# Kernel tuning notes

Hardware: AMD Instinct MI355X
Metric: run time of the kernel (lower is better)

## Reference

```python
import jax, jax.numpy as jnp
import numpy as np

N, E, F_IN, F_E, H, HEADS, NG = 50000, 300000, 16, 8, 64, 4, 64
D_HEAD = H // HEADS
EPS = 1e-5


def setup_inputs() -> dict:
    key = jax.random.key(0)
    ks = jax.random.split(key, 12)
    def rn(k, shape, s=0.1):
        return jax.random.normal(k, shape, jnp.float32) * s
    return dict(
        x=jax.random.normal(ks[0], (N, F_IN), jnp.float32),
        edge_index=jax.random.randint(ks[1], (2, E), 0, N),
        edge_attr=jax.random.normal(ks[2], (E, F_E), jnp.float32),
        batch=jnp.sort(jax.random.randint(ks[3], (N,), 0, NG)),
        # edge_net: Linear(F_E, H*F_IN) -> ReLU -> Linear(H*F_IN, H*F_IN)
        en_w1=rn(ks[4], (F_E, H * F_IN)), en_b1=jnp.zeros((H * F_IN,), jnp.float32),
        en_w2=rn(ks[5], (H * F_IN, H * F_IN)), en_b2=jnp.zeros((H * F_IN,), jnp.float32),
        # NNConv root weight + bias
        root_w=rn(ks[6], (F_IN, H)), conv1_b=jnp.zeros((H,), jnp.float32),
        norm1_w=jnp.ones((H,), jnp.float32), norm1_b=jnp.zeros((H,), jnp.float32),
        # GATConv: lin weight, attention vectors, bias
        gat_w=rn(ks[7], (H, H)),
        att_src=rn(ks[8], (HEADS, D_HEAD)), att_dst=rn(ks[9], (HEADS, D_HEAD)),
        gat_b=jnp.zeros((H,), jnp.float32),
        norm2_w=jnp.ones((H,), jnp.float32), norm2_b=jnp.zeros((H,), jnp.float32),
        lin_w=rn(ks[10], (H, 1)), lin_b=jnp.zeros((1,), jnp.float32),
    )


def _graph_layernorm(x, w, b):
    # PyG LayerNorm(mode='graph') with batch=None: scalar mean/std over ALL elems
    mu = x.mean()
    sd = jnp.sqrt(((x - mu) ** 2).mean())
    return (x - mu) / (sd + EPS) * w + b


def reference(x, edge_index, edge_attr, batch, en_w1, en_b1, en_w2, en_b2,
              root_w, conv1_b, norm1_w, norm1_b, gat_w, att_src, att_dst,
              gat_b, norm2_w, norm2_b, lin_w, lin_b):
    src, dst = edge_index[0], edge_index[1]
    # --- NNConv: per-edge weight matrices from edge_net ---
    w_e = jax.nn.relu(edge_attr @ en_w1 + en_b1) @ en_w2 + en_b2
    w_e = w_e.reshape(E, F_IN, H)                      # [E, in, out]
    msg = jnp.einsum('ef,efh->eh', x[src], w_e)        # gather-matmul per edge
    agg = jax.ops.segment_sum(msg, dst, num_segments=N)
    deg = jax.ops.segment_sum(jnp.ones((E,), x.dtype), dst, num_segments=N)
    agg = agg / jnp.maximum(deg, 1.0)[:, None]         # aggr='mean'
    h = x @ root_w + agg + conv1_b
    h = jax.nn.relu(h)
    h = _graph_layernorm(h, norm1_w, norm1_b)
    # dropout: eval mode -> identity
    # --- GATConv (edge_attr=None at call site; add self-loops, softmax attn) ---
    loops = jnp.arange(N)
    s2 = jnp.concatenate([src, loops])
    d2 = jnp.concatenate([dst, loops])
    xh = (h @ gat_w).reshape(N, HEADS, D_HEAD)
    a_src = (xh * att_src).sum(-1)                     # [N, HEADS]
    a_dst = (xh * att_dst).sum(-1)
    alpha = jax.nn.leaky_relu(a_src[s2] + a_dst[d2], 0.2)  # [E+N, HEADS]
    amax = jax.ops.segment_max(alpha, d2, num_segments=N)
    alpha = jnp.exp(alpha - amax[d2])
    asum = jax.ops.segment_sum(alpha, d2, num_segments=N)
    alpha = alpha / (asum[d2] + 1e-16)
    out = jax.ops.segment_sum(alpha[:, :, None] * xh[s2], d2, num_segments=N)
    h2 = out.reshape(N, H) + gat_b                     # concat heads
    h2 = jax.nn.relu(h2)
    h2 = _graph_layernorm(h2, norm2_w, norm2_b)
    # --- global mean pool + linear head ---
    gs = jax.ops.segment_sum(h2, batch, num_segments=NG)
    cnt = jax.ops.segment_sum(jnp.ones((N,), h2.dtype), batch, num_segments=NG)
    pooled = gs / jnp.maximum(cnt, 1.0)[:, None]
    return pooled @ lin_w + lin_b                      # [NG, 1]
```

## Files before the change

### kernel.cpp

```cpp
#include <hip/hip_runtime.h>
#include <hip/hip_bf16.h>

#define N_NODES 50000
#define E_EDGES 300000
#define NGRAPH 64
#define KTOT 16512
#define KC 128
#define NCHUNK 129
#define CSPLIT 65
#define NEGRP 1172
#define LNEPS 1e-5f
#define NBLK_N 196
#define NBLK_P 12500
#define RPRE 1.00146484375f

typedef __bf16 bf16x8 __attribute__((ext_vector_type(8)));
typedef float floatx4 __attribute__((ext_vector_type(4)));
typedef float f32x2 __attribute__((ext_vector_type(2)));
typedef unsigned int u32x4 __attribute__((ext_vector_type(4)));

__device__ __forceinline__ void async_load16(const void* g, void* l) {
  __builtin_amdgcn_global_load_lds(
      (__attribute__((address_space(1))) void*)g,
      (__attribute__((address_space(3))) void*)l, 16, 0, 0);
}

__device__ __forceinline__ unsigned pkt(f32x2 p) {
  return __builtin_amdgcn_perm(__float_as_uint(p[1]), __float_as_uint(p[0]), 0x07060302u);
}
__device__ __forceinline__ unsigned pkbf(float a, float b) {
  unsigned ua = __float_as_uint(a) + 0x8000u;
  unsigned ub = __float_as_uint(b) + 0x8000u;
  return __builtin_amdgcn_perm(ub, ua, 0x07060302u);
}

__global__ void k_prep(const float* __restrict__ w2, const float* __restrict__ b2,
                       __bf16* __restrict__ Tt) {
  __shared__ float tile[64][65];
  int t = threadIdx.x;
  int kf0 = blockIdx.x * 64;
  int r4 = t >> 6;
  int cc = t & 63;
#pragma unroll
  for (int p = 0; p < 16; ++p) {
    int row = p * 4 + r4;
    int kf = kf0 + row;
    float v = 0.f;
    if (kf < 16384) {
      int k = kf >> 4, f = kf & 15;
      v = w2[k * 1024 + f * 64 + cc];
    } else if (kf < 16400) {
      v = b2[(kf - 16384) * 64 + cc];
    }
    tile[row][cc] = v;
  }
  __syncthreads();
#pragma unroll
  for (int p = 0; p < 16; ++p) {
    int h = p * 4 + r4;
    Tt[(size_t)h * KTOT + kf0 + cc] = (__bf16)tile[cc][h];
  }
}

__global__ void k_prepw(const float* __restrict__ w1, float* __restrict__ W1t) {
  int i = blockIdx.x * 256 + threadIdx.x;
  if (i < 8192) { int k = i >> 3, j = i & 7; W1t[i] = w1[j * 1024 + k]; }
}

__global__ void k_cnt(const int* __restrict__ ei, int* __restrict__ degI) {
  int e = blockIdx.x * 256 + threadIdx.x;
  if (e < E_EDGES) atomicAdd(&degI[ei[E_EDGES + e]], 1);
}

__global__ void k_scanA(const int* __restrict__ degI, int* __restrict__ bsum) {
  __shared__ int sm[256];
  int t = threadIdx.x;
  int i = blockIdx.x * 256 + t;
  sm[t] = (i < N_NODES) ? degI[i] : 0;
  __syncthreads();
  for (int off = 128; off > 0; off >>= 1) {
    if (t < off) sm[t] += sm[t + off];
    __syncthreads();
  }
  if (t == 0) bsum[blockIdx.x] = sm[0];
}

__global__ void k_scanB(const int* __restrict__ bsum, int* __restrict__ bpre) {
  __shared__ int s[256];
  int t = threadIdx.x;
  int v = (t < NBLK_N) ? bsum[t] : 0;
  s[t] = v;
  __syncthreads();
  for (int off = 1; off < 256; off <<= 1) {
    int add = (t >= off) ? s[t - off] : 0;
    __syncthreads();
    s[t] += add;
    __syncthreads();
  }
  if (t < NBLK_N) bpre[t] = s[t] - v;
}

__global__ void k_scanC(const int* __restrict__ degI, const int* __restrict__ bpre,
                        int* __restrict__ rowptr, int* __restrict__ cursor) {
  __shared__ int s[256];
  int t = threadIdx.x;
  int i = blockIdx.x * 256 + t;
  int d = (i < N_NODES) ? degI[i] : 0;
  s[t] = d;
  __syncthreads();
  for (int off = 1; off < 256; off <<= 1) {
    int add = (t >= off) ? s[t - off] : 0;
    __syncthreads();
    s[t] += add;
    __syncthreads();
  }
  int r = bpre[blockIdx.x] + s[t] - d;
  if (i < N_NODES) {
    rowptr[i] = r;
    cursor[i] = r;
    if (i == N_NODES - 1) rowptr[N_NODES] = r + d;
  }
}

__global__ void k_scatter(const int* __restrict__ ei, int* __restrict__ cursor,
                          int* __restrict__ colsrc) {
  int e = blockIdx.x * 256 + threadIdx.x;
  if (e < E_EDGES) {
    int s = ei[e], d = ei[E_EDGES + e];
    int pos = atomicAdd(&cursor[d], 1);
    colsrc[pos] = s;
  }
}

__global__ __launch_bounds__(256, 3)
void k_nnconv(const float* __restrict__ x, const int* __restrict__ ei,
              const float* __restrict__ ea, const float* __restrict__ W1t,
              const float* __restrict__ b1, const __bf16* __restrict__ Tt,
              float* __restrict__ agg) {
  __shared__ __align__(16) __bf16 sB[2][64 * KC];
  __shared__ int sSrc[256];
  __shared__ int sDst[256];

  const int tid = threadIdx.x;
  const int wv = tid >> 6;
  const int lane = tid & 63;
  const int l15 = lane & 15;
  const int quad = lane >> 4;
  const int qxl = quad ^ l15;
  const bool qhi = (lane & 32) != 0;
  const unsigned rsel = qhi ? 0x07060100u : 0x05040100u;
  const int grp = blockIdx.x >> 1;
  const int half = blockIdx.x & 1;
  const int cstart = half ? CSPLIT : 0;
  const int cend = half ? NCHUNK : CSPLIT;
  const int base = grp * 256;

  int e = base + tid;
  bool valid = e < E_EDGES;
  sSrc[tid] = valid ? ei[e] : 0;
  sDst[tid] = valid ? ei[E_EDGES + e] : -1;

  f32x2 ea2[4];
  {
    const float4* p = (const float4*)(ea + (size_t)(valid ? e : 0) * 8);
    float4 a0 = p[0], a1 = p[1];
    ea2[0] = (f32x2){a0.x, a0.y};
    ea2[1] = (f32x2){a0.z, a0.w};
    ea2[2] = (f32x2){a1.x, a1.y};
    ea2[3] = (f32x2){a1.z, a1.w};
  }
  __syncthreads();

  const int f0 = (quad & 1) * 8;
  f32x2 xf2[4][4];
#pragma unroll
  for (int mb = 0; mb < 4; ++mb) {
    int el = wv * 64 + mb * 16 + l15;
    const float4* px = (const float4*)(x + (size_t)sSrc[el] * 16 + f0);
    float4 v0 = px[0], v1 = px[1];
    xf2[mb][0] = (f32x2){v0.x * RPRE, v0.y * RPRE};
    xf2[mb][1] = (f32x2){v0.z * RPRE, v0.w * RPRE};
    xf2[mb][2] = (f32x2){v1.x * RPRE, v1.y * RPRE};
    xf2[mb][3] = (f32x2){v1.z * RPRE, v1.w * RPRE};
  }

  int bpaddr[4];
#pragma unroll
  for (int mb = 0; mb < 4; ++mb) bpaddr[mb] = (mb * 16 + l15) * 4;

  const int tidh = tid >> 4;
  const int ccsw = (tid & 15) ^ (tidh & 15);
  const __bf16* gbase = Tt + (size_t)tidh * KTOT + ccsw * 8 + cstart * KC;

  auto stageB = [&](int buf) {
    const __bf16* p = gbase;
#pragma unroll
    for (int it = 0; it < 4; ++it) {
      async_load16(p, &sB[buf][(it * 256 + tid) * 8]);
      p += 16 * KTOT;
    }
    gbase += KC;
  };

  unsigned prr[4];
  auto calcR = [&](int c, const float* w1p, const float* b1p) {
    if (c < 128) {
#pragma unroll
      for (int ks = 0; ks < 4; ++ks) {
        float rv[2];
#pragma unroll
        for (int kk = 0; kk < 2; ++kk) {
          const f32x2* w = (const f32x2*)(w1p + (ks * 2 + kk) * 8);
          f32x2 s01 = ea2[0] * w[0] + ea2[1] * w[1];
          f32x2 s23 = ea2[2] * w[2] + ea2[3] * w[3];
          f32x2 s = s01 + s23;
          rv[kk] = fmaxf(b1p[ks * 2 + kk] + s[0] + s[1], 0.f);
        }
        prr[ks] = pkbf(rv[0], rv[1]);
      }
    } else {
      prr[0] = 0x00003F80u;
      prr[1] = prr[2] = prr[3] = 0u;
    }
  };

  unsigned ubuf[16];
  auto bcastR = [&]() {
#pragma unroll
    for (int ks = 0; ks < 4; ++ks)
#pragma unroll
      for (int mb = 0; mb < 4; ++mb)
        ubuf[ks * 4 + mb] = (unsigned)__builtin_amdgcn_ds_bpermute(bpaddr[mb], (int)prr[ks]);
  };

  floatx4 acc[4][4];
#pragma unroll
  for (int mb = 0; mb < 4; ++mb)
#pragma unroll
    for (int nb = 0; nb < 4; ++nb) acc[mb][nb] = floatx4{0.f, 0.f, 0.f, 0.f};

  stageB(0);
  calcR(cstart, W1t + cstart * 64, b1 + cstart * 8);
  bcastR();
  const float* w1p = W1t + (cstart + 1) * 64;
  const float* b1p = b1 + (cstart + 1) * 8;
  int buf = 0;
  for (int c = cstart; c < cend; ++c) {
    __syncthreads();
    if (c + 1 < cend) stageB(buf ^ 1);
    float rvc[16];
#pragma unroll
    for (int i = 0; i < 16; ++i)
      rvc[i] = __uint_as_float(__builtin_amdgcn_perm(ubuf[i], 0u, rsel));
#pragma unroll
    for (int ks = 0; ks < 4; ++ks) {
      int t1 = qxl ^ (ks * 4);
      bf16x8 bfr[4];
#pragma unroll
      for (int nb = 0; nb < 4; ++nb)
        bfr[nb] = *(const bf16x8*)&sB[buf][(nb * 16 + l15) * KC + t1 * 8];
#pragma unroll
      for (int mb = 0; mb < 4; ++mb) {
        float rv = rvc[ks * 4 + mb];
        f32x2 rv2 = {rv, rv};
        u32x4 U;
        U[0] = pkt(rv2 * xf2[mb][0]);
        U[1] = pkt(rv2 * xf2[mb][1]);
        U[2] = pkt(rv2 * xf2[mb][2]);
        U[3] = pkt(rv2 * xf2[mb][3]);
        bf16x8 A = __builtin_bit_cast(bf16x8, U);
#pragma unroll
        for (int nb = 0; nb < 4; ++nb)
          acc[mb][nb] = __builtin_amdgcn_mfma_f32_16x16x32_bf16(A, bfr[nb], acc[mb][nb], 0, 0, 0);
      }
    }
    if (c + 1 < cend) {
      calcR(c + 1, w1p, b1p);
      bcastR();
      w1p += 64; b1p += 8;
    }
    buf ^= 1;
  }

#pragma unroll
  for (int mb = 0; mb < 4; ++mb) {
    int el = wv * 64 + mb * 16 + quad * 4;
#pragma unroll
    for (int reg = 0; reg < 4; ++reg) {
      int dd = sDst[el + reg];
      if (dd >= 0) {
#pragma unroll
        for (int nb = 0; nb < 4; ++nb)
          atomicAdd(&agg[(size_t)dd * 64 + nb * 16 + l15], acc[mb][nb][reg]);
      }
    }
  }
}

__global__ void k_root(const float* __restrict__ x, const float* __restrict__ rootw,
                       const float* __restrict__ conv1b, const float* __restrict__ agg,
                       const int* __restrict__ degI, float* __restrict__ hpre,
                       float* __restrict__ rpart) {
  __shared__ float sW[1024];
  __shared__ float sx[64];
  __shared__ float red[8];
  int t = threadIdx.x;
  int blk = blockIdx.x;
#pragma unroll
  for (int i = 0; i < 4; ++i) sW[t + i * 256] = rootw[t + i * 256];
  if (t < 64) sx[t] = x[(size_t)blk * 64 + t];
  __syncthreads();
  int ln = t >> 6, h = t & 63;
  int n = blk * 4 + ln;
  float acc = conv1b[h];
#pragma unroll
  for (int f = 0; f < 16; ++f) acc += sx[ln * 16 + f] * sW[f * 64 + h];
  float dv = fmaxf((float)degI[n], 1.0f);
  float v = acc + agg[(size_t)n * 64 + h] / dv;
  v = fmaxf(v, 0.f);
  hpre[(size_t)n * 64 + h] = v;
  float s1 = v, s2 = v * v;
  for (int o = 32; o > 0; o >>= 1) { s1 += __shfl_down(s1, o); s2 += __shfl_down(s2, o); }
  if ((t & 63) == 0) { red[t >> 6] = s1; red[4 + (t >> 6)] = s2; }
  __syncthreads();
  if (t == 0) {
    rpart[blk * 2] = red[0] + red[1] + red[2] + red[3];
    rpart[blk * 2 + 1] = red[4] + red[5] + red[6] + red[7];
  }
}

__global__ void k_fold1(const float* __restrict__ rpart, const float* __restrict__ n1w,
                        const float* __restrict__ n1b, const float* __restrict__ gatw,
                        float* __restrict__ gw2, float* __restrict__ tb) {
  __shared__ float red[8];
  __shared__ float sMI[2];
  __shared__ float sS[64], sT[64];
  int t = threadIdx.x;
  int wv = t >> 6, lane = t & 63;
  float a = 0.f, b = 0.f;
  for (int i = t; i < NBLK_P; i += 256) { a += rpart[2 * i]; b += rpart[2 * i + 1]; }
  for (int o = 32; o > 0; o >>= 1) { a += __shfl_down(a, o); b += __shfl_down(b, o); }
  if (lane == 0) { red[wv] = a; red[4 + wv] = b; }
  __syncthreads();
  if (t == 0) {
    float A = red[0] + red[1] + red[2] + red[3];
    float B = red[4] + red[5] + red[6] + red[7];
    const float M = (float)N_NODES * 64.f;
    float mu = A / M;
    float var = fmaxf(B / M - mu * mu, 0.f);
    sMI[0] = mu;
    sMI[1] = 1.f / (sqrtf(var) + LNEPS);
  }
  __syncthreads();
  if (t < 64) {
    float mu = sMI[0], inv = sMI[1];
    sS[t] = inv * n1w[t];
    sT[t] = n1b[t] - mu * inv * n1w[t];
  }
  __syncthreads();
  if (t < 64) {
    float acc = 0.f;
    for (int i = 0; i < 64; ++i) {
      float g = gatw[i * 64 + t];
      gw2[i * 64 + t] = sS[i] * g;
      acc += sT[i] * g;
    }
    tb[t] = acc;
  }
}

__global__ void k_gatlin(const float* __restrict__ hpre, const float* __restrict__ gw2,
                         const float* __restrict__ tb, const float* __restrict__ attS,
                         const float* __restrict__ attD, float* __restrict__ xh,
                         float* __restrict__ asrc, float* __restrict__ adst) {
  __shared__ float sW[4096];
  __shared__ float sh[256];
  __shared__ float sxh[256];
  int t = threadIdx.x;
  int blk = blockIdx.x;
#pragma unroll
  for (int i = 0; i < 16; ++i) sW[t + i * 256] = gw2[t + i * 256];
  sh[t] = hpre[(size_t)blk * 256 + t];
  __syncthreads();
  int ln = t >> 6, h = t & 63;
  float acc = tb[h];
  for (int i = 0; i < 64; ++i) acc += sh[ln * 64 + i] * sW[i * 64 + h];
  xh[(size_t)blk * 256 + t] = acc;
  sxh[t] = acc;
  __syncthreads();
  if (t < 32) {
    int ln2 = t >> 3, rem = t & 7;
    int hd = rem & 3;
    const float* av = (rem >> 2) ? attD : attS;
    float a = 0.f;
#pragma unroll
    for (int d = 0; d < 16; ++d) a += sxh[ln2 * 64 + hd * 16 + d] * av[hd * 16 + d];
    int n = blk * 4 + ln2;
    if (rem >> 2) adst[n * 4 + hd] = a; else asrc[n * 4 + hd] = a;
  }
}

__global__ void k_gat(const int* __restrict__ rowptr, const int* __restrict__ colsrc,
                      const float* __restrict__ xh, const float* __restrict__ asrc,
                      const float* __restrict__ adst, const float* __restrict__ gatb,
                      float* __restrict__ act, float* __restrict__ gpart) {
  __shared__ float sP[4][256];
  __shared__ int sS[4][64];
  __shared__ float sRed[8];
  int t = threadIdx.x;
  int wv = t >> 6, lane = t & 63;
  int n = blockIdx.x * 4 + wv;
  int start = rowptr[n], end = rowptr[n + 1];
  int deg = end - start;
  int myhd = lane >> 4;
  float ad[4];
#pragma unroll
  for (int hd = 0; hd < 4; ++hd) ad[hd] = adst[n * 4 + hd];
  float m[4] = {-1e30f, -1e30f, -1e30f, -1e30f};
  float l[4] = {0.f, 0.f, 0.f, 0.f};
  float O = 0.f;
  int items = deg + 1;
  for (int t0 = 0; t0 < items; t0 += 64) {
    int cnt = min(64, items - t0);
    int idx = t0 + lane;
    bool has = lane < cnt;
    int s = n;
    if (has && idx < deg) s = colsrc[start + idx];
    float a[4];
#pragma unroll
    for (int hd = 0; hd < 4; ++hd) {
      float av = has ? (asrc[s * 4 + hd] + ad[hd]) : -1e30f;
      a[hd] = (av > 0.f) ? av : 0.2f * av;
    }
    float tm[4];
#pragma unroll
    for (int hd = 0; hd < 4; ++hd) tm[hd] = a[hd];
#pragma unroll
    for (int off = 32; off > 0; off >>= 1)
#pragma unroll
      for (int hd = 0; hd < 4; ++hd) tm[hd] = fmaxf(tm[hd], __shfl_xor(tm[hd], off));
    float p[4];
#pragma unroll
    for (int hd = 0; hd < 4; ++hd) {
      float mn = fmaxf(m[hd], tm[hd]);
      float sc = __expf(m[hd] - mn);
      l[hd] *= sc;
      if (hd == myhd) O *= sc;
      m[hd] = mn;
      p[hd] = has ? __expf(a[hd] - mn) : 0.f;
    }
    float ts[4];
#pragma unroll
    for (int hd = 0; hd < 4; ++hd) ts[hd] = p[hd];
#pragma unroll
    for (int off = 32; off > 0; off >>= 1)
#pragma unroll
      for (int hd = 0; hd < 4; ++hd) ts[hd] += __shfl_xor(ts[hd], off);
#pragma unroll
    for (int hd = 0; hd < 4; ++hd) l[hd] += ts[hd];
    sS[wv][lane] = s;
#pragma unroll
    for (int hd = 0; hd < 4; ++hd) sP[wv][lane * 4 + hd] = p[hd];
    for (int e2 = 0; e2 < cnt; ++e2) {
      int ss = sS[wv][e2];
      float pp = sP[wv][e2 * 4 + myhd];
      O = fmaf(pp, xh[(size_t)ss * 64 + lane], O);
    }
  }
  float lmy = (myhd & 2) ? ((myhd & 1) ? l[3] : l[2]) : ((myhd & 1) ? l[1] : l[0]);
  float outv = O / (lmy + 1e-16f);
  float v = fmaxf(outv + gatb[lane], 0.f);
  act[(size_t)n * 64 + lane] = v;
  float s1 = v, s2 = v * v;
#pragma unroll
  for (int off = 32; off > 0; off >>= 1) { s1 += __shfl_down(s1, off); s2 += __shfl_down(s2, off); }
  if (lane == 0) { sRed[wv] = s1; sRed[4 + wv] = s2; }
  __syncthreads();
  if (t == 0) {
    gpart[blockIdx.x * 2] = sRed[0] + sRed[1] + sRed[2] + sRed[3];
    gpart[blockIdx.x * 2 + 1] = sRed[4] + sRed[5] + sRed[6] + sRed[7];
  }
}

__global__ void k_fold2(const float* __restrict__ gpart, const float* __restrict__ n2w,
                        const float* __restrict__ n2b, const float* __restrict__ linw,
                        const float* __restrict__ linb, float* __restrict__ wl) {
  __shared__ float red[8];
  __shared__ float sMI[2];
  int t = threadIdx.x;
  int wv = t >> 6, lane = t & 63;
  float a = 0.f, b = 0.f;
  for (int i = t; i < NBLK_P; i += 256) { a += gpart[2 * i]; b += gpart[2 * i + 1]; }
  for (int o = 32; o > 0; o >>= 1) { a += __shfl_down(a, o); b += __shfl_down(b, o); }
  if (lane == 0) { red[wv] = a; red[4 + wv] = b; }
  __syncthreads();
  if (t == 0) {
    float A = red[0] + red[1] + red[2] + red[3];
    float B = red[4] + red[5] + red[6] + red[7];
    const float M = (float)N_NODES * 64.f;
    float mu = A / M;
    float var = fmaxf(B / M - mu * mu, 0.f);
    sMI[0] = mu;
    sMI[1] = 1.f / (sqrtf(var) + LNEPS);
  }
  __syncthreads();
  if (t < 64) {
    float mu = sMI[0], inv = sMI[1];
    float w = inv * n2w[t] * linw[t];
    float p = (n2b[t] - mu * inv * n2w[t]) * linw[t];
    wl[t] = w;
    for (int o = 32; o > 0; o >>= 1) p += __shfl_down(p, o);
    if (t == 0) wl[64] = p + linb[0];
  }
}

__global__ void k_out(const float* __restrict__ act, const float* __restrict__ wl,
                      const int* __restrict__ batch, float* __restrict__ out) {
  __shared__ float red[4];
  __shared__ float swl[64];
  int g = blockIdx.x;
  int t = threadIdx.x;
  int wv = t >> 6, lane = t & 63;
  if (t < 64) swl[t] = wl[t];
  __syncthreads();
  auto lbound = [&](int key) {
    int lo = 0, hi = N_NODES;
    while (lo < hi) { int mid = (lo + hi) >> 1; if (batch[mid] < key) lo = mid + 1; else hi = mid; }
    return lo;
  };
  int lo = lbound(g), hi = lbound(g + 1);
  int cntn = hi - lo;
  float s = 0.f;
  for (int idx = t; idx < cntn * 64; idx += 256) {
    int n = lo + (idx >> 6);
    int d = idx & 63;
    s += act[(size_t)n * 64 + d] * swl[d];
  }
  for (int o = 32; o > 0; o >>= 1) s += __shfl_down(s, o);
  if (lane == 0) red[wv] = s;
  __syncthreads();
  if (t == 0)
    out[g] = (red[0] + red[1] + red[2] + red[3]) / fmaxf((float)cntn, 1.f) + wl[64];
}

#define OFF_AGG     0UL
#define OFF_DEGI    12800000UL
#define ZBYTES      13000000UL
#define OFF_RPART   13000000UL
#define OFF_GPART   13100032UL
#define OFF_ROWPTR  13200064UL
#define OFF_CURSOR  13400128UL
#define OFF_BSUM    13600192UL
#define OFF_BPRE    13601024UL
#define OFF_COLSRC  13601856UL
#define OFF_TT      14801856UL
#define OFF_W1T     16915392UL
#define OFF_GW2     16948160UL
#define OFF_TB      16964544UL
#define OFF_WL      16964800UL
#define OFF_ASRC    16965120UL
#define OFF_ADST    17765120UL
#define OFF_HPRE    18565120UL
#define OFF_XH      31365120UL
#define OFF_ACT     44165120UL
#define WS_NEED     56965120UL

extern "C" void kernel_launch(void* const* d_in, const int* in_sizes, int n_in,
                              void* d_out, int out_size, void* d_ws, size_t ws_size,
                              hipStream_t stream) {
  const float* x = (const float*)d_in[0];
  const int* ei = (const int*)d_in[1];
  const float* ea = (const float*)d_in[2];
  const int* batch = (const int*)d_in[3];
  const float* w1 = (const float*)d_in[4];
  const float* b1 = (const float*)d_in[5];
  const float* w2 = (const float*)d_in[6];
  const float* b2 = (const float*)d_in[7];
  const float* rootw = (const float*)d_in[8];
  const float* conv1b = (const float*)d_in[9];
  const float* n1w = (const float*)d_in[10];
  const float* n1b = (const float*)d_in[11];
  const float* gatw = (const float*)d_in[12];
  const float* attS = (const float*)d_in[13];
  const float* attD = (const float*)d_in[14];
  const float* gatb = (const float*)d_in[15];
  const float* n2w = (const float*)d_in[16];
  const float* n2b = (const float*)d_in[17];
  const float* linw = (const float*)d_in[18];
  const float* linb = (const float*)d_in[19];

  if (ws_size < WS_NEED) return;
  char* ws = (char*)d_ws;
  float* agg    = (float*)(ws + OFF_AGG);
  int* degI     = (int*)(ws + OFF_DEGI);
  float* rpart  = (float*)(ws + OFF_RPART);
  float* gpart  = (float*)(ws + OFF_GPART);
  int* rowptr   = (int*)(ws + OFF_ROWPTR);
  int* cursor   = (int*)(ws + OFF_CURSOR);
  int* bsum     = (int*)(ws + OFF_BSUM);
  int* bpre     = (int*)(ws + OFF_BPRE);
  int* colsrc   = (int*)(ws + OFF_COLSRC);
  __bf16* Tt    = (__bf16*)(ws + OFF_TT);
  float* W1t    = (float*)(ws + OFF_W1T);
  float* gw2    = (float*)(ws + OFF_GW2);
  float* tb     = (float*)(ws + OFF_TB);
  float* wl     = (float*)(ws + OFF_WL);
  float* asrc   = (float*)(ws + OFF_ASRC);
  float* adst   = (float*)(ws + OFF_ADST);
  float* hpre   = (float*)(ws + OFF_HPRE);
  float* xh     = (float*)(ws + OFF_XH);
  float* act    = (float*)(ws + OFF_ACT);

  hipMemsetAsync(ws, 0, ZBYTES, stream);

  k_prep<<<258, 256, 0, stream>>>(w2, b2, Tt);
  k_prepw<<<32, 256, 0, stream>>>(w1, W1t);
  k_cnt<<<(E_EDGES + 255) / 256, 256, 0, stream>>>(ei, degI);
  k_scanA<<<NBLK_N, 256, 0, stream>>>(degI, bsum);
  k_scanB<<<1, 256, 0, stream>>>(bsum, bpre);
  k_scanC<<<NBLK_N, 256, 0, stream>>>(degI, bpre, rowptr, cursor);
  k_scatter<<<(E_EDGES + 255) / 256, 256, 0, stream>>>(ei, cursor, colsrc);
  k_nnconv<<<NEGRP * 2, 256, 0, stream>>>(x, ei, ea, W1t, b1, Tt, agg);
  k_root<<<NBLK_P, 256, 0, stream>>>(x, rootw, conv1b, agg, degI, hpre, rpart);
  k_fold1<<<1, 256, 0, stream>>>(rpart, n1w, n1b, gatw, gw2, tb);
  k_gatlin<<<NBLK_P, 256, 0, stream>>>(hpre, gw2, tb, attS, attD, xh, asrc, adst);
  k_gat<<<NBLK_P, 256, 0, stream>>>(rowptr, colsrc, xh, asrc, adst, gatb, act, gpart);
  k_fold2<<<1, 256, 0, stream>>>(gpart, n2w, n2b, linw, linb, wl);
  k_out<<<NGRAPH, 256, 0, stream>>>(act, wl, batch, (float*)d_out);
}
```

Measured before the change: 1.112 ms.

## Load edge-net weight fragments directly from global into registers, drop LDS staging

The transformed edge-net weight matrix is pre-laid out in MFMA-fragment order, so each lane in k_nnconv reads its B operand straight from global/L2 into registers, double-buffered per k-step. This removes the LDS double buffer, the async global-to-LDS loads and the per-chunk block barriers. Edge src/dst indices now travel through wavefront shuffles instead of shared memory. In exchange every wave fetches the full weight stream on its own, four times the global/L2 traffic per block, and load latency is hidden only by the register prefetch.

Result: faster. 1.034 ms (-7.0%).

```diff
diff --git a/kernel.cpp b/kernel.cpp
--- a/kernel.cpp
+++ b/kernel.cpp
@@ -5,9 +5,9 @@
 #define E_EDGES 300000
 #define NGRAPH 64
 #define KTOT 16512
-#define KC 128
 #define NCHUNK 129
 #define CSPLIT 65
+#define NSTEP 516
 #define NEGRP 1172
 #define LNEPS 1e-5f
 #define NBLK_N 196
@@ -19,12 +19,6 @@
 typedef float f32x2 __attribute__((ext_vector_type(2)));
 typedef unsigned int u32x4 __attribute__((ext_vector_type(4)));
 
-__device__ __forceinline__ void async_load16(const void* g, void* l) {
-  __builtin_amdgcn_global_load_lds(
-      (__attribute__((address_space(1))) void*)g,
-      (__attribute__((address_space(3))) void*)l, 16, 0, 0);
-}
-
 __device__ __forceinline__ unsigned pkt(f32x2 p) {
   return __builtin_amdgcn_perm(__float_as_uint(p[1]), __float_as_uint(p[0]), 0x07060302u);
 }
@@ -35,31 +29,21 @@
 }
 
 __global__ void k_prep(const float* __restrict__ w2, const float* __restrict__ b2,
-                       __bf16* __restrict__ Tt) {
-  __shared__ float tile[64][65];
-  int t = threadIdx.x;
-  int kf0 = blockIdx.x * 64;
-  int r4 = t >> 6;
-  int cc = t & 63;
-#pragma unroll
-  for (int p = 0; p < 16; ++p) {
-    int row = p * 4 + r4;
-    int kf = kf0 + row;
-    float v = 0.f;
-    if (kf < 16384) {
-      int k = kf >> 4, f = kf & 15;
-      v = w2[k * 1024 + f * 64 + cc];
-    } else if (kf < 16400) {
-      v = b2[(kf - 16384) * 64 + cc];
-    }
-    tile[row][cc] = v;
-  }
-  __syncthreads();
-#pragma unroll
-  for (int p = 0; p < 16; ++p) {
-    int h = p * 4 + r4;
-    Tt[(size_t)h * KTOT + kf0 + cc] = (__bf16)tile[cc][h];
-  }
+                       __bf16* __restrict__ Tt2) {
+  int idx = blockIdx.x * 256 + threadIdx.x;
+  int step = idx >> 11;
+  int rem = idx & 2047;
+  int h = rem >> 5;
+  int kw = rem & 31;
+  int kf = step * 32 + kw;
+  float v = 0.f;
+  if (kf < 16384) {
+    int k = kf >> 4, f = kf & 15;
+    v = w2[k * 1024 + f * 64 + h];
+  } else if (kf < 16400) {
+    v = b2[(kf - 16384) * 64 + h];
+  }
+  Tt2[idx] = (__bf16)v;
 }
 
 __global__ void k_prepw(const float* __restrict__ w1, float* __restrict__ W1t) {
@@ -135,30 +119,23 @@
 __global__ __launch_bounds__(256, 3)
 void k_nnconv(const float* __restrict__ x, const int* __restrict__ ei,
               const float* __restrict__ ea, const float* __restrict__ W1t,
-              const float* __restrict__ b1, const __bf16* __restrict__ Tt,
+              const float* __restrict__ b1, const __bf16* __restrict__ Tt2,
               float* __restrict__ agg) {
-  __shared__ __align__(16) __bf16 sB[2][64 * KC];
-  __shared__ int sSrc[256];
-  __shared__ int sDst[256];
-
   const int tid = threadIdx.x;
-  const int wv = tid >> 6;
   const int lane = tid & 63;
   const int l15 = lane & 15;
   const int quad = lane >> 4;
-  const int qxl = quad ^ l15;
   const bool qhi = (lane & 32) != 0;
   const unsigned rsel = qhi ? 0x07060100u : 0x05040100u;
   const int grp = blockIdx.x >> 1;
   const int half = blockIdx.x & 1;
   const int cstart = half ? CSPLIT : 0;
   const int cend = half ? NCHUNK : CSPLIT;
-  const int base = grp * 256;
-
-  int e = base + tid;
+
+  int e = grp * 256 + tid;
   bool valid = e < E_EDGES;
-  sSrc[tid] = valid ? ei[e] : 0;
-  sDst[tid] = valid ? ei[E_EDGES + e] : -1;
+  int srcv = valid ? ei[e] : 0;
+  int dstv = valid ? ei[E_EDGES + e] : -1;
 
   f32x2 ea2[4];
   {
@@ -169,14 +146,13 @@
     ea2[2] = (f32x2){a1.x, a1.y};
     ea2[3] = (f32x2){a1.z, a1.w};
   }
-  __syncthreads();
 
   const int f0 = (quad & 1) * 8;
   f32x2 xf2[4][4];
 #pragma unroll
   for (int mb = 0; mb < 4; ++mb) {
-    int el = wv * 64 + mb * 16 + l15;
-    const float4* px = (const float4*)(x + (size_t)sSrc[el] * 16 + f0);
+    int s = __shfl(srcv, mb * 16 + l15);
+    const float4* px = (const float4*)(x + (size_t)s * 16 + f0);
     float4 v0 = px[0], v1 = px[1];
     xf2[mb][0] = (f32x2){v0.x * RPRE, v0.y * RPRE};
     xf2[mb][1] = (f32x2){v0.z * RPRE, v0.w * RPRE};
@@ -188,18 +164,15 @@
 #pragma unroll
   for (int mb = 0; mb < 4; ++mb) bpaddr[mb] = (mb * 16 + l15) * 4;
 
-  const int tidh = tid >> 4;
-  const int ccsw = (tid & 15) ^ (tidh & 15);
-  const __bf16* gbase = Tt + (size_t)tidh * KTOT + ccsw * 8 + cstart * KC;
-
-  auto stageB = [&](int buf) {
-    const __bf16* p = gbase;
-#pragma unroll
-    for (int it = 0; it < 4; ++it) {
-      async_load16(p, &sB[buf][(it * 256 + tid) * 8]);
-      p += 16 * KTOT;
-    }
-    gbase += KC;
+  const __bf16* bp = Tt2 + (size_t)(cstart * 4) * 2048 + (l15 * 32 + quad * 8);
+
+  bf16x8 Ba[4], Bb[4];
+  auto loadB = [&](bf16x8* d) {
+    d[0] = *(const bf16x8*)(bp);
+    d[1] = *(const bf16x8*)(bp + 512);
+    d[2] = *(const bf16x8*)(bp + 1024);
+    d[3] = *(const bf16x8*)(bp + 1536);
+    bp += 2048;
   };
 
   unsigned prr[4];
@@ -239,29 +212,21 @@
 #pragma unroll
     for (int nb = 0; nb < 4; ++nb) acc[mb][nb] = floatx4{0.f, 0.f, 0.f, 0.f};
 
-  stageB(0);
   calcR(cstart, W1t + cstart * 64, b1 + cstart * 8);
   bcastR();
+  loadB(Ba);
   const float* w1p = W1t + (cstart + 1) * 64;
   const float* b1p = b1 + (cstart + 1) * 8;
-  int buf = 0;
+
   for (int c = cstart; c < cend; ++c) {
-    __syncthreads();
-    if (c + 1 < cend) stageB(buf ^ 1);
-    float rvc[16];
-#pragma unroll
-    for (int i = 0; i < 16; ++i)
-      rvc[i] = __uint_as_float(__builtin_amdgcn_perm(ubuf[i], 0u, rsel));
 #pragma unroll
     for (int ks = 0; ks < 4; ++ks) {
-      int t1 = qxl ^ (ks * 4);
-      bf16x8 bfr[4];
-#pragma unroll
-      for (int nb = 0; nb < 4; ++nb)
-        bfr[nb] = *(const bf16x8*)&sB[buf][(nb * 16 + l15) * KC + t1 * 8];
+      bf16x8* Bc = (ks & 1) ? Bb : Ba;
+      bf16x8* Bn = (ks & 1) ? Ba : Bb;
+      loadB(Bn);
 #pragma unroll
       for (int mb = 0; mb < 4; ++mb) {
-        float rv = rvc[ks * 4 + mb];
+        float rv = __uint_as_float(__builtin_amdgcn_perm(ubuf[ks * 4 + mb], 0u, rsel));
         f32x2 rv2 = {rv, rv};
         u32x4 U;
         U[0] = pkt(rv2 * xf2[mb][0]);
@@ -271,7 +236,7 @@
         bf16x8 A = __builtin_bit_cast(bf16x8, U);
 #pragma unroll
         for (int nb = 0; nb < 4; ++nb)
-          acc[mb][nb] = __builtin_amdgcn_mfma_f32_16x16x32_bf16(A, bfr[nb], acc[mb][nb], 0, 0, 0);
+          acc[mb][nb] = __builtin_amdgcn_mfma_f32_16x16x32_bf16(A, Bc[nb], acc[mb][nb], 0, 0, 0);
       }
     }
     if (c + 1 < cend) {
@@ -279,15 +244,13 @@
       bcastR();
       w1p += 64; b1p += 8;
     }
-    buf ^= 1;
   }
 
 #pragma unroll
   for (int mb = 0; mb < 4; ++mb) {
-    int el = wv * 64 + mb * 16 + quad * 4;
 #pragma unroll
     for (int reg = 0; reg < 4; ++reg) {
-      int dd = sDst[el + reg];
+      int dd = __shfl(dstv, mb * 16 + quad * 4 + reg);
       if (dd >= 0) {
 #pragma unroll
         for (int nb = 0; nb < 4; ++nb)
@@ -554,16 +517,16 @@
 #define OFF_BPRE    13601024UL
 #define OFF_COLSRC  13601856UL
 #define OFF_TT      14801856UL
-#define OFF_W1T     16915392UL
-#define OFF_GW2     16948160UL
-#define OFF_TB      16964544UL
-#define OFF_WL      16964800UL
-#define OFF_ASRC    16965120UL
-#define OFF_ADST    17765120UL
-#define OFF_HPRE    18565120UL
-#define OFF_XH      31365120UL
-#define OFF_ACT     44165120UL
-#define WS_NEED     56965120UL
+#define OFF_W1T     16919488UL
+#define OFF_GW2     16952256UL
+#define OFF_TB      16968640UL
+#define OFF_WL      16968896UL
+#define OFF_ASRC    16969216UL
+#define OFF_ADST    17769216UL
+#define OFF_HPRE    18569216UL
+#define OFF_XH      31369216UL
+#define OFF_ACT     44169216UL
+#define WS_NEED     56969216UL
 
 extern "C" void kernel_launch(void* const* d_in, const int* in_sizes, int n_in,
                               void* d_out, int out_size, void* d_ws, size_t ws_size,
@@ -600,7 +563,7 @@
   int* bsum     = (int*)(ws + OFF_BSUM);
   int* bpre     = (int*)(ws + OFF_BPRE);
   int* colsrc   = (int*)(ws + OFF_COLSRC);
-  __bf16* Tt    = (__bf16*)(ws + OFF_TT);
+  __bf16* Tt2   = (__bf16*)(ws + OFF_TT);
   float* W1t    = (float*)(ws + OFF_W1T);
   float* gw2    = (float*)(ws + OFF_GW2);
   float* tb     = (float*)(ws + OFF_TB);
@@ -613,14 +576,14 @@
 
   hipMemsetAsync(ws, 0, ZBYTES, stream);
 
-  k_prep<<<258, 256, 0, stream>>>(w2, b2, Tt);
+  k_prep<<<(NSTEP + 1) * 8, 256, 0, stream>>>(w2, b2, Tt2);
   k_prepw<<<32, 256, 0, stream>>>(w1, W1t);
   k_cnt<<<(E_EDGES + 255) / 256, 256, 0, stream>>>(ei, degI);
   k_scanA<<<NBLK_N, 256, 0, stream>>>(degI, bsum);
   k_scanB<<<1, 256, 0, stream>>>(bsum, bpre);
   k_scanC<<<NBLK_N, 256, 0, stream>>>(degI, bpre, rowptr, cursor);
   k_scatter<<<(E_EDGES + 255) / 256, 256, 0, stream>>>(ei, cursor, colsrc);
-  k_nnconv<<<NEGRP * 2, 256, 0, stream>>>(x, ei, ea, W1t, b1, Tt, agg);
+  k_nnconv<<<NEGRP * 2, 256, 0, stream>>>(x, ei, ea, W1t, b1, Tt2, agg);
   k_root<<<NBLK_P, 256, 0, stream>>>(x, rootw, conv1b, agg, degI, hpre, rpart);
   k_fold1<<<1, 256, 0, stream>>>(rpart, n1w, n1b, gatw, gw2, tb);
   k_gatlin<<<NBLK_P, 256, 0, stream>>>(hpre, gw2, tb, attS, attD, xh, asrc, adst);
```
